# Kernel tuning notes

Hardware: AMD Instinct MI355X
Metric: run time of the kernel (lower is better)

The kernel has to match this reference:

```python
import jax, jax.numpy as jnp
import numpy as np

D_MODEL = 512; D_STATE = 128; D_CONV = 4; EXPAND = 2; HEADDIM = 64; CHUNK = 64
D_INNER = EXPAND * D_MODEL            # 1024
NHEADS = D_INNER // HEADDIM           # 16
CONV_DIM = D_INNER + 2 * D_STATE      # 1280
D_IN_PROJ = 2 * D_INNER + 2 * D_STATE + NHEADS  # 2320
BATCH, SEQLEN = 2, 8192


def setup_inputs() -> dict:
    key = jax.random.key(0)
    ks = jax.random.split(key, 8)
    s = 0.02
    return {
        "x": jax.random.normal(ks[0], (BATCH, SEQLEN, D_MODEL), jnp.float32),
        "in_proj_w": jax.random.normal(ks[1], (D_IN_PROJ, D_MODEL), jnp.float32) * s,
        "conv_w": jax.random.normal(ks[2], (CONV_DIM, 1, D_CONV), jnp.float32) * s,
        "conv_b": jnp.zeros((CONV_DIM,), jnp.float32),
        "dt_bias": jax.random.normal(ks[3], (NHEADS,), jnp.float32) * s,
        "A_log": jnp.log(jnp.arange(1, NHEADS + 1, dtype=jnp.float32)),
        "D_skip": jnp.ones((NHEADS,), jnp.float32),
        "norm_w": jnp.ones((D_INNER,), jnp.float32),
        "ssm_out_w": jax.random.normal(ks[4], (D_MODEL, D_INNER), jnp.float32) * s,
        "fuse_w": jax.random.normal(ks[5], (D_MODEL, 2 * D_MODEL), jnp.float32) * s,
        "fuse_b": jnp.zeros((D_MODEL,), jnp.float32),
    }


def segsum(a):
    # a: (..., T) -> (..., T, T) with [i, j] = sum_{j < d <= i} a[d]; -inf above diag
    T = a.shape[-1]
    a = jnp.broadcast_to(a[..., :, None], a.shape + (T,))
    a = jnp.where(jnp.tril(jnp.ones((T, T), bool), -1), a, 0.0)
    a = jnp.cumsum(a, axis=-2)
    return jnp.where(jnp.tril(jnp.ones((T, T), bool), 0), a, -jnp.inf)


def ssd(x, A, B, C):
    # x: (b,l,h,p), A: (b,l,h), B/C: (b,l,n) (single group, broadcast over heads)
    b, l, h, p = x.shape
    c = l // CHUNK
    x = x.reshape(b, c, CHUNK, h, p)
    A = jnp.transpose(A.reshape(b, c, CHUNK, h), (0, 3, 1, 2))   # (b,h,c,s)
    B = B.reshape(b, c, CHUNK, -1)
    C = C.reshape(b, c, CHUNK, -1)
    A_cumsum = jnp.cumsum(A, axis=-1)                             # (b,h,c,s)
    L = jnp.exp(segsum(A))                                        # (b,h,c,s,s) intra-chunk decay
    Y_diag = jnp.einsum("bcln,bcsn,bhcls,bcshp->bclhp", C, B, L, x)
    decay_states = jnp.exp(A_cumsum[..., -1:] - A_cumsum)         # (b,h,c,s)
    states = jnp.einsum("bcln,bhcl,bclhp->bchpn", B, decay_states, x)
    init = jnp.zeros_like(states[:, :1])
    A_pad = jnp.pad(A_cumsum[..., -1], ((0, 0), (0, 0), (1, 0)))  # (b,h,c+1)
    decay_chunk = jnp.exp(segsum(A_pad))                          # (b,h,c+1,c+1)
    new_states = jnp.einsum("bhzc,bchpn->bzhpn", decay_chunk,
                            jnp.concatenate([init, states], axis=1))
    states = new_states[:, :-1]                                   # state entering each chunk
    state_decay_out = jnp.exp(A_cumsum)
    Y_off = jnp.einsum("bchpn,bcsn,bhcs->bcshp", states, C, state_decay_out)
    return (Y_diag + Y_off).reshape(b, l, h, p)


def mamba2_block(u, in_proj_w, conv_w, conv_b, dt_bias, A_log, D_skip, norm_w, ssm_out_w):
    b, l, _ = u.shape
    zxbcdt = u @ in_proj_w.T                                      # (b,l,2320)
    z = zxbcdt[..., :D_INNER]
    xBC = zxbcdt[..., D_INNER:D_INNER + CONV_DIM]
    dt = jax.nn.softplus(zxbcdt[..., -NHEADS:] + dt_bias)         # (b,l,h)
    # depthwise causal conv over time
    conv = jax.lax.conv_general_dilated(
        jnp.transpose(xBC, (0, 2, 1)), conv_w, (1,), [(D_CONV - 1, 0)],
        dimension_numbers=("NCH", "OIH", "NCH"), feature_group_count=CONV_DIM)
    xBC = jax.nn.silu(jnp.transpose(conv + conv_b[None, :, None], (0, 2, 1)))
    xh = xBC[..., :D_INNER].reshape(b, l, NHEADS, HEADDIM)
    Bm = xBC[..., D_INNER:D_INNER + D_STATE]
    Cm = xBC[..., -D_STATE:]
    A = -jnp.exp(A_log)                                           # (h,)
    y = ssd(xh * dt[..., None], A * dt, Bm, Cm)
    y = y + xh * D_skip[None, None, :, None]
    y = y.reshape(b, l, D_INNER)
    # gated RMSNorm
    y = y * jax.nn.silu(z)
    y = y * jax.lax.rsqrt(jnp.mean(y * y, axis=-1, keepdims=True) + 1e-5) * norm_w
    return y @ ssm_out_w.T


def reference(x, in_proj_w, conv_w, conv_b, dt_bias, A_log, D_skip, norm_w,
              ssm_out_w, fuse_w, fuse_b):
    args = (in_proj_w, conv_w, conv_b, dt_bias, A_log, D_skip, norm_w, ssm_out_w)
    y_fwd = mamba2_block(x, *args)
    y_rev = jnp.flip(mamba2_block(jnp.flip(x, 1), *args), 1)
    y_cat = jnp.concatenate([y_fwd, y_rev], axis=-1)
    return y_cat @ fuse_w.T + fuse_b
```

## Files before the change

### kernel.cpp

```cpp
#include <hip/hip_runtime.h>
#include <cstddef>

#define B_SZ     2
#define L_SEQ    8192
#define D_INNERC 1024
#define NHEADSC  16
#define CHUNKC   64
#define NCHUNKC  128
#define CONV_DIMC 1280
#define D_PROJC  2320
#define M_ROWS   16384

typedef unsigned short bfu;

using bf16x8 = __attribute__((ext_vector_type(8))) short;
using f32x4  = __attribute__((ext_vector_type(4))) float;

__device__ __forceinline__ float silu_(float v) { return v / (1.f + expf(-v)); }

__device__ __forceinline__ float b2f(bfu u) {
  return __uint_as_float((unsigned)u << 16);
}
__device__ __forceinline__ bfu f2b(float f) {
  unsigned x = __float_as_uint(f);
  return (bfu)((x + 0x7fffu + ((x >> 16) & 1u)) >> 16);
}

__device__ __forceinline__ float4 ld4(const float* p) { return *(const float4*)p; }
__device__ __forceinline__ float4 ld4(const bfu* p) {
  ushort4 u = *(const ushort4*)p;
  float4 f;
  f.x = b2f(u.x); f.y = b2f(u.y); f.z = b2f(u.z); f.w = b2f(u.w);
  return f;
}
__device__ __forceinline__ void st4(float* p, float4 v) { *(float4*)p = v; }
__device__ __forceinline__ void st4(bfu* p, float4 v) {
  ushort4 u;
  u.x = f2b(v.x); u.y = f2b(v.y); u.z = f2b(v.z); u.w = f2b(v.w);
  *(ushort4*)p = u;
}

__device__ __forceinline__ void gl_lds16(const bfu* g, bfu* l) {
  __builtin_amdgcn_global_load_lds(
      (const __attribute__((address_space(1))) unsigned int*)g,
      (__attribute__((address_space(3))) unsigned int*)l, 16, 0, 0);
}

__device__ __forceinline__ int pos_of(int b, int c, int l, int dir) {
  int t = c * CHUNKC + l;
  return dir ? (b * L_SEQ + (L_SEQ - 1) - t) : (b * L_SEQ + t);
}

__global__ __launch_bounds__(256)
void mfma_nt(const bfu* __restrict__ A, int lda,
             const bfu* __restrict__ Bw, int ldb,
             void* __restrict__ Cv, int ldc,
             int N, int K, const float* __restrict__ bias, int mode)
{
  __shared__ bfu sh[16384];
  bfu* As = sh;
  bfu* Bs = sh + 8192;
  const int tid  = threadIdx.x;
  const int lane = tid & 63;
  const int wave = __builtin_amdgcn_readfirstlane(tid >> 6);
  const int wm = wave & 1, wn = wave >> 1;

  const int num_n = gridDim.x;
  const int flat  = blockIdx.y * num_n + blockIdx.x;
  const int xcd   = flat & 7;
  const int g     = flat >> 3;
  const int n0 = (g % num_n) * 128;
  const int m0 = ((g / num_n) * 8 + xcd) * 128;

  f32x4 acc[4][4];
#pragma unroll
  for (int i = 0; i < 4; ++i)
#pragma unroll
    for (int j = 0; j < 4; ++j)
      acc[i][j] = (f32x4){0.f, 0.f, 0.f, 0.f};

  const int ro   = lane >> 3;
  const int slot = lane & 7;

  for (int k0 = 0; k0 < K; k0 += 64) {
    __syncthreads();
#pragma unroll
    for (int si = 0; si < 4; ++si) {
      int r = wave * 32 + si * 8 + ro;
      int cg = slot ^ (r & 7);
      gl_lds16(A  + (size_t)(m0 + r) * lda + k0 + cg * 8, As + (wave * 32 + si * 8) * 64);
      gl_lds16(Bw + (size_t)(n0 + r) * ldb + k0 + cg * 8, Bs + (wave * 32 + si * 8) * 64);
    }
    __syncthreads();

#pragma unroll
    for (int ks = 0; ks < 2; ++ks) {
      bf16x8 af[4], bfr[4];
#pragma unroll
      for (int i = 0; i < 4; ++i) {
        int ra = wm * 64 + i * 16 + (lane & 15);
        int ca = (ks * 4 + (lane >> 4)) ^ (ra & 7);
        af[i] = *(const bf16x8*)(As + ra * 64 + ca * 8);
        int rb = wn * 64 + i * 16 + (lane & 15);
        int cb = (ks * 4 + (lane >> 4)) ^ (rb & 7);
        bfr[i] = *(const bf16x8*)(Bs + rb * 64 + cb * 8);
      }
#pragma unroll
      for (int i = 0; i < 4; ++i)
#pragma unroll
        for (int j = 0; j < 4; ++j)
          acc[i][j] = __builtin_amdgcn_mfma_f32_16x16x32_bf16(af[i], bfr[j], acc[i][j], 0, 0, 0);
    }
  }

  __syncthreads();
  if (mode == 0) {
#pragma unroll
    for (int i = 0; i < 4; ++i)
#pragma unroll
      for (int j = 0; j < 4; ++j)
#pragma unroll
        for (int r = 0; r < 4; ++r) {
          int ml = wm * 64 + i * 16 + (lane >> 4) * 4 + r;
          int nl = wn * 64 + j * 16 + (lane & 15);
          sh[ml * 128 + nl] = f2b(acc[i][j][r]);
        }
    __syncthreads();
    bfu* Cb = (bfu*)Cv;
#pragma unroll
    for (int rr = 0; rr < 8; ++rr) {
      int idx = rr * 256 + tid;
      int row = idx >> 4, co = (idx & 15) * 8;
      if (n0 + co < N) {
        *(ulonglong2*)(Cb + (size_t)(m0 + row) * ldc + n0 + co) =
            *(const ulonglong2*)(sh + row * 128 + co);
      }
    }
  } else {
    float* Cf = (float*)Cv;
    float* shf = (float*)sh;
#pragma unroll
    for (int p = 0; p < 2; ++p) {
      if (wm == p) {
#pragma unroll
        for (int i = 0; i < 4; ++i)
#pragma unroll
          for (int j = 0; j < 4; ++j)
#pragma unroll
            for (int r = 0; r < 4; ++r) {
              int ml = i * 16 + (lane >> 4) * 4 + r;
              int nl = wn * 64 + j * 16 + (lane & 15);
              shf[ml * 128 + nl] = acc[i][j][r];
            }
      }
      __syncthreads();
#pragma unroll
      for (int rr = 0; rr < 8; ++rr) {
        int idx = rr * 256 + tid;
        int row = idx >> 5, co = (idx & 31) * 4;
        int n = n0 + co;
        if (n < N) {
          float4 v = *(float4*)(shf + row * 128 + co);
          float* cp = Cf + (size_t)(m0 + p * 64 + row) * ldc + n;
          if (mode == 2) {
            float4 o = *(float4*)cp;
            v.x += o.x; v.y += o.y; v.z += o.z; v.w += o.w;
          } else if (bias) {
            v.x += bias[n]; v.y += bias[n + 1]; v.z += bias[n + 2]; v.w += bias[n + 3];
          }
          *(float4*)cp = v;
        }
      }
      __syncthreads();
    }
  }
}

__global__ __launch_bounds__(256)
void cvt_x_k(const float* __restrict__ in, bfu* __restrict__ out)
{
  int q = blockIdx.x * 256 + threadIdx.x;
  st4(out + (size_t)q * 4, ld4(in + (size_t)q * 4));
}

__global__ __launch_bounds__(256)
void cvt_w_k(const float* __restrict__ in, bfu* __restrict__ out)
{
  int q = blockIdx.x * 256 + threadIdx.x;
  int row = q >> 7, c4 = (q & 127) << 2;
  float4 v = {0.f, 0.f, 0.f, 0.f};
  if (row < D_PROJC) v = ld4(in + (size_t)row * 512 + c4);
  st4(out + (size_t)row * 512 + c4, v);
}

__global__ __launch_bounds__(256)
void transpose_k(const float* __restrict__ in, bfu* __restrict__ out)
{
  int idx = blockIdx.x * 256 + threadIdx.x;
  int j = idx >> 9, k = idx & 511;
  out[idx] = f2b(in[k * 1024 + j]);
}

__global__ __launch_bounds__(256)
void cvt_fuse_k(const float* __restrict__ in, bfu* __restrict__ out)
{
  int q = blockIdx.x * 256 + threadIdx.x;
  int m = q >> 7, kg = (q & 127) << 2;
  float4 v = ld4(in + (size_t)(m & 511) * 1024 + (m >> 9) * 512 + kg);
  st4(out + (size_t)m * 512 + kg, v);
}

__global__ __launch_bounds__(256)
void conv_k(const bfu* __restrict__ zx, const float* __restrict__ conv_w,
            const float* __restrict__ conv_b, bfu* __restrict__ xBC, int dir)
{
  int ch = blockIdx.x * 256 + threadIdx.x;
  int m0 = blockIdx.y * 8;
  int b  = m0 >> 13, tb = m0 & (L_SEQ - 1);
  float w0 = conv_w[ch * 4 + 0], w1 = conv_w[ch * 4 + 1];
  float w2 = conv_w[ch * 4 + 2], w3 = conv_w[ch * 4 + 3];
  float cb = conv_b[ch];
  const bfu* src = zx + 1024 + ch;
  const int shift = dir ? 0 : 3;

  float v[11];
#pragma unroll
  for (int i = 0; i < 11; ++i) {
    int tt = tb + i - shift;
    v[i] = (tt >= 0 && tt < L_SEQ)
         ? b2f(src[(size_t)(b * L_SEQ + tt) * D_PROJC]) : 0.f;
  }
#pragma unroll
  for (int j = 0; j < 8; ++j) {
    float acc = cb;
    if (dir == 0) {
      acc += w0 * v[j] + w1 * v[j + 1] + w2 * v[j + 2] + w3 * v[j + 3];
    } else {
      acc += w0 * v[j + 3] + w1 * v[j + 2] + w2 * v[j + 1] + w3 * v[j];
    }
    xBC[(size_t)(m0 + j) * CONV_DIMC + ch] = f2b(silu_(acc));
  }
}

__global__ __launch_bounds__(256)
void states_mfma_k(const bfu* __restrict__ zx, const bfu* __restrict__ xBC,
                   const float* __restrict__ dt_bias, const float* __restrict__ A_log,
                   float* __restrict__ acum_g, float* __restrict__ dt_g,
                   bfu* __restrict__ states, int dir)
{
  __shared__ bfu BT[128 * 72];
  __shared__ bfu xsT[64 * 72];
  __shared__ float scaleS[8 * 64];

  int bid = blockIdx.x;
  int hb = bid >> 8;
  int c = bid & 127, b = (bid >> 7) & 1;
  int tid = threadIdx.x, lane = tid & 63;
  int w = tid >> 6, q = lane >> 4, t = lane & 15;

#pragma unroll
  for (int rr = 0; rr < 2; ++rr) {
    int i = w + rr * 4;
    int h = hb * 8 + i;
    int l = lane;
    int pos = pos_of(b, c, l, dir);
    float dtr = b2f(zx[(size_t)pos * D_PROJC + 2304 + h]) + dt_bias[h];
    float dt = (dtr > 20.f) ? dtr : log1pf(expf(dtr));
    float a = -expf(A_log[h]) * dt;
#pragma unroll
    for (int off = 1; off < 64; off <<= 1) {
      float v = __shfl_up(a, off);
      if (l >= off) a += v;
    }
    float alast = __shfl(a, 63);
    int gi = ((b * NCHUNKC + c) * NHEADSC + h) * 64 + l;
    acum_g[gi] = a; dt_g[gi] = dt;
    scaleS[i * 64 + l] = dt * expf(alast - a);
  }

#pragma unroll
  for (int r = 0; r < 8; ++r) {
    int qq = tid + r * 256;
    int l = qq & 63, ng = qq >> 6;
    ushort4 v = *(const ushort4*)(xBC + (size_t)pos_of(b, c, l, dir) * CONV_DIMC + 1024 + ng * 4);
    BT[(ng * 4 + 0) * 72 + l] = v.x; BT[(ng * 4 + 1) * 72 + l] = v.y;
    BT[(ng * 4 + 2) * 72 + l] = v.z; BT[(ng * 4 + 3) * 72 + l] = v.w;
  }
  __syncthreads();

  for (int i = 0; i < 8; ++i) {
    int h = hb * 8 + i;
#pragma unroll
    for (int r = 0; r < 4; ++r) {
      int qq = tid + r * 256;
      int l = qq & 63, pg = qq >> 6;
      float s = scaleS[i * 64 + l];
      ushort4 v = *(const ushort4*)(xBC + (size_t)pos_of(b, c, l, dir) * CONV_DIMC + h * 64 + pg * 4);
      xsT[(pg * 4 + 0) * 72 + l] = f2b(b2f(v.x) * s);
      xsT[(pg * 4 + 1) * 72 + l] = f2b(b2f(v.y) * s);
      xsT[(pg * 4 + 2) * 72 + l] = f2b(b2f(v.z) * s);
      xsT[(pg * 4 + 3) * 72 + l] = f2b(b2f(v.w) * s);
    }
    __syncthreads();

    bf16x8 axs[2];
#pragma unroll
    for (int ks = 0; ks < 2; ++ks)
      axs[ks] = *(const bf16x8*)(xsT + (w * 16 + t) * 72 + ks * 32 + q * 8);

    f32x4 acc[8];
#pragma unroll
    for (int j = 0; j < 8; ++j) acc[j] = (f32x4){0.f, 0.f, 0.f, 0.f};
#pragma unroll
    for (int ks = 0; ks < 2; ++ks)
#pragma unroll
      for (int j = 0; j < 8; ++j) {
        bf16x8 bB = *(const bf16x8*)(BT + (j * 16 + t) * 72 + ks * 32 + q * 8);
        acc[j] = __builtin_amdgcn_mfma_f32_16x16x32_bf16(axs[ks], bB, acc[j], 0, 0, 0);
      }

    size_t base = ((size_t)(b * NCHUNKC + c) * NHEADSC + h) * 8192;
#pragma unroll
    for (int j = 0; j < 8; ++j)
#pragma unroll
      for (int r = 0; r < 4; ++r) {
        int p = w * 16 + q * 4 + r, n = j * 16 + t;
        states[base + p * 128 + n] = f2b(acc[j][r]);
      }
    __syncthreads();
  }
}

__global__ __launch_bounds__(256)
void scan_k(bfu* __restrict__ states, const float* __restrict__ acum_g)
{
  int bid = blockIdx.x;
  int eb = bid & 15, h = (bid >> 4) & 15, b = bid >> 8;
  int e = eb * 512 + threadIdx.x * 2;
  bfu* p0 = states + ((size_t)(b * NCHUNKC) * NHEADSC + h) * 8192 + e;
  const float* ac = acum_g + ((b * NCHUNKC) * NHEADSC + h) * 64 + 63;
  const size_t cstride = (size_t)NHEADSC * 8192;
  const int astride = NHEADSC * 64;

  float pre0 = 0.f, pre1 = 0.f;
  uint raw = *(const uint*)p0;
  float dcur = expf(ac[0]);
  for (int c = 0; c < NCHUNKC; ++c) {
    uint raw_next = 0; float dnext = 0.f;
    if (c < NCHUNKC - 1) {
      raw_next = *(const uint*)(p0 + (c + 1) * cstride);
      dnext = expf(ac[(c + 1) * astride]);
    }
    float v0 = b2f((bfu)(raw & 0xffff));
    float v1 = b2f((bfu)(raw >> 16));
    uint packed = (uint)f2b(pre0) | ((uint)f2b(pre1) << 16);
    *(uint*)(p0 + c * cstride) = packed;
    pre0 = v0 + dcur * pre0;
    pre1 = v1 + dcur * pre1;
    raw = raw_next; dcur = dnext;
  }
}

__global__ __launch_bounds__(256)
void y_mfma_k(const bfu* __restrict__ xBC, const bfu* __restrict__ states,
              const float* __restrict__ acum_g, const float* __restrict__ dt_g,
              const float* __restrict__ D_skip, bfu* __restrict__ ybuf, int dir)
{
  __shared__ bfu smem[30976];
  bfu* Cs  = smem;
  bfu* Bsc = smem + 8704;
  bfu* Ps  = smem + 17408;
  bfu* xhT = smem + 26112;
  float* acumH = (float*)(smem + 30720);
  float* dtH   = acumH + 64;

  int bid = blockIdx.x;
  int hb = bid >> 8;
  int c = bid & 127, b = (bid >> 7) & 1;
  int tid = threadIdx.x, lane = tid & 63;
  int w = tid >> 6, q = lane >> 4, t = lane & 15;

#pragma unroll
  for (int r = 0; r < 8; ++r) {
    int qq = tid + r * 256;
    int row = qq >> 5, grp = qq & 31;
    const bfu* src = xBC + (size_t)pos_of(b, c, row, dir) * CONV_DIMC;
    *(ushort4*)(Cs  + row * 136 + grp * 4) = *(const ushort4*)(src + 1152 + grp * 4);
    *(ushort4*)(Bsc + row * 136 + grp * 4) = *(const ushort4*)(src + 1024 + grp * 4);
  }
  __syncthreads();

  bf16x8 af[4];
#pragma unroll
  for (int ks = 0; ks < 4; ++ks)
    af[ks] = *(const bf16x8*)(Cs + (w * 16 + t) * 136 + ks * 32 + q * 8);

  f32x4 sacc[4];
#pragma unroll
  for (int j = 0; j < 4; ++j) sacc[j] = (f32x4){0.f, 0.f, 0.f, 0.f};
#pragma unroll
  for (int ks = 0; ks < 4; ++ks)
#pragma unroll
    for (int j = 0; j < 4; ++j) {
      bf16x8 bf = *(const bf16x8*)(Bsc + (j * 16 + t) * 136 + ks * 32 + q * 8);
      sacc[j] = __builtin_amdgcn_mfma_f32_16x16x32_bf16(af[ks], bf, sacc[j], 0, 0, 0);
    }

  for (int i = 0; i < 8; ++i) {
    int h = hb * 8 + i;
    __syncthreads();
    size_t pbase = ((size_t)(b * NCHUNKC + c) * NHEADSC + h) * 8192;
#pragma unroll
    for (int r = 0; r < 8; ++r) {
      int qq = tid + r * 256;
      int row = qq >> 5, grp = qq & 31;
      *(ushort4*)(Ps + row * 136 + grp * 4) =
          *(const ushort4*)(states + pbase + row * 128 + grp * 4);
    }
#pragma unroll
    for (int r = 0; r < 4; ++r) {
      int qq = tid + r * 256;
      int l = qq & 63, pg = qq >> 6;
      ushort4 v = *(const ushort4*)(xBC + (size_t)pos_of(b, c, l, dir) * CONV_DIMC + h * 64 + pg * 4);
      xhT[(pg * 4 + 0) * 72 + l] = v.x; xhT[(pg * 4 + 1) * 72 + l] = v.y;
      xhT[(pg * 4 + 2) * 72 + l] = v.z; xhT[(pg * 4 + 3) * 72 + l] = v.w;
    }
    if (tid < 64) {
      int gi = ((b * NCHUNKC + c) * NHEADSC + h) * 64 + tid;
      acumH[tid] = acum_g[gi]; dtH[tid] = dt_g[gi];
    }
    __syncthreads();

    f32x4 yacc[4];
#pragma unroll
    for (int j = 0; j < 4; ++j) yacc[j] = (f32x4){0.f, 0.f, 0.f, 0.f};
#pragma unroll
    for (int ks = 0; ks < 4; ++ks)
#pragma unroll
      for (int j = 0; j < 4; ++j) {
        bf16x8 bP = *(const bf16x8*)(Ps + (j * 16 + t) * 136 + ks * 32 + q * 8);
        yacc[j] = __builtin_amdgcn_mfma_f32_16x16x32_bf16(af[ks], bP, yacc[j], 0, 0, 0);
      }

    float Dh = D_skip[h];
    bfu* sc = Bsc;
#pragma unroll
    for (int j = 0; j < 4; ++j)
#pragma unroll
      for (int r = 0; r < 4; ++r) {
        int l = w * 16 + q * 4 + r, s = j * 16 + t;
        float v = 0.f;
        if (s <= l) v = sacc[j][r] * expf(acumH[l] - acumH[s]) * dtH[s];
        if (s == l) v += Dh;
        sc[l * 72 + s] = f2b(v);
      }

    f32x4 acc2[4];
    float dec[4];
#pragma unroll
    for (int r = 0; r < 4; ++r) dec[r] = expf(acumH[w * 16 + q * 4 + r]);
#pragma unroll
    for (int j = 0; j < 4; ++j)
#pragma unroll
      for (int r = 0; r < 4; ++r) acc2[j][r] = yacc[j][r] * dec[r];

#pragma unroll
    for (int ks = 0; ks < 2; ++ks) {
      bf16x8 asc = *(const bf16x8*)(sc + (w * 16 + t) * 72 + ks * 32 + q * 8);
#pragma unroll
      for (int j = 0; j < 4; ++j) {
        bf16x8 bx = *(const bf16x8*)(xhT + (j * 16 + t) * 72 + ks * 32 + q * 8);
        acc2[j] = __builtin_amdgcn_mfma_f32_16x16x32_bf16(asc, bx, acc2[j], 0, 0, 0);
      }
    }

#pragma unroll
    for (int j = 0; j < 4; ++j)
#pragma unroll
      for (int r = 0; r < 4; ++r) {
        int l = w * 16 + q * 4 + r, p = j * 16 + t;
        ybuf[(size_t)pos_of(b, c, l, dir) * D_INNERC + h * 64 + p] = f2b(acc2[j][r]);
      }
  }
}

__global__ __launch_bounds__(256)
void norm_k(bfu* __restrict__ ybuf, const bfu* __restrict__ zx,
            const float* __restrict__ norm_w)
{
  int m = blockIdx.x, tid = threadIdx.x;
  float4 y = ld4(ybuf + (size_t)m * D_INNERC + tid * 4);
  float4 z = ld4(zx + (size_t)m * D_PROJC + tid * 4);
  float4 g;
  g.x = y.x * silu_(z.x); g.y = y.y * silu_(z.y);
  g.z = y.z * silu_(z.z); g.w = y.w * silu_(z.w);
  float ss = g.x * g.x + g.y * g.y + g.z * g.z + g.w * g.w;
#pragma unroll
  for (int off = 32; off >= 1; off >>= 1) ss += __shfl_xor(ss, off);
  __shared__ float red[4];
  int wid = tid >> 6;
  if ((tid & 63) == 0) red[wid] = ss;
  __syncthreads();
  float tot = red[0] + red[1] + red[2] + red[3];
  float scale = rsqrtf(tot * (1.f / 1024.f) + 1e-5f);
  float4 w = *(const float4*)(norm_w + tid * 4);
  g.x *= scale * w.x; g.y *= scale * w.y; g.z *= scale * w.z; g.w *= scale * w.w;
  st4(ybuf + (size_t)m * D_INNERC + tid * 4, g);
}

extern "C" void kernel_launch(void* const* d_in, const int* in_sizes, int n_in,
                              void* d_out, int out_size, void* d_ws, size_t ws_size,
                              hipStream_t stream)
{
  const float* x         = (const float*)d_in[0];
  const float* in_proj_w = (const float*)d_in[1];
  const float* conv_w    = (const float*)d_in[2];
  const float* conv_b    = (const float*)d_in[3];
  const float* dt_bias   = (const float*)d_in[4];
  const float* A_log     = (const float*)d_in[5];
  const float* D_skip    = (const float*)d_in[6];
  const float* norm_w    = (const float*)d_in[7];
  const float* ssm_out_w = (const float*)d_in[8];
  const float* fuse_w    = (const float*)d_in[9];
  const float* fuse_b    = (const float*)d_in[10];
  float* out = (float*)d_out;

  bfu* zx     = (bfu*)d_ws;
  bfu* xBC    = zx     + (size_t)M_ROWS * D_PROJC;
  bfu* states = xBC    + (size_t)M_ROWS * CONV_DIMC;
  bfu* ybuf   = states + (size_t)33554432;
  float* acum = (float*)(ybuf + (size_t)M_ROWS * D_INNERC);
  float* dtg  = acum + 262144;
  bfu* ssmTb  = (bfu*)(dtg + 262144);
  bfu* fuseA  = ssmTb + 524288;
  bfu* wcmb   = fuseA + 524288;
  bfu* xb = states;
  bfu* wb = states + 8388608;

  cvt_x_k<<<8192, 256, 0, stream>>>(x, xb);
  cvt_w_k<<<1216, 256, 0, stream>>>(in_proj_w, wb);
  transpose_k<<<2048, 256, 0, stream>>>(ssm_out_w, ssmTb);
  cvt_fuse_k<<<512, 256, 0, stream>>>(fuse_w, fuseA);

  mfma_nt<<<dim3(8, 8), 256, 0, stream>>>(
      fuseA, 512, ssmTb, 512, wcmb, 1024, 1024, 512, nullptr, 0);

  mfma_nt<<<dim3(19, 128), 256, 0, stream>>>(
      xb, 512, wb, 512, zx, D_PROJC, D_PROJC, 512, nullptr, 0);

  for (int dir = 0; dir < 2; ++dir) {
    conv_k<<<dim3(5, 2048), 256, 0, stream>>>(zx, conv_w, conv_b, xBC, dir);
    states_mfma_k<<<512, 256, 0, stream>>>(zx, xBC, dt_bias, A_log, acum, dtg, states, dir);
    scan_k<<<512, 256, 0, stream>>>(states, acum);
    y_mfma_k<<<512, 256, 0, stream>>>(xBC, states, acum, dtg, D_skip, ybuf, dir);
    norm_k<<<M_ROWS, 256, 0, stream>>>(ybuf, zx, norm_w);
    mfma_nt<<<dim3(4, 128), 256, 0, stream>>>(
        ybuf, 1024, wcmb + (size_t)dir * 524288, 1024, out, 512,
        512, 1024, dir == 0 ? fuse_b : nullptr, dir == 0 ? 1 : 2);
  }
}
```

Before: 528.7 us.

## Add 256x256-tile 8-wave pipelined MFMA GEMM for the input projection

Adds a new 512-thread GEMM kernel with 256x256 output tiles, double-buffered LDS staging via direct global-to-LDS loads, XOR-swizzled layout, and interleaved load/compute phases with explicit waitcnt and barriers. It also remaps blocks across the XCDs. The in_proj GEMM now uses this kernel, and the weight conversion is padded to 2560 rows so the 256-wide N tiles stay in bounds. The aim is more reuse per block and better overlap of memory traffic with MFMA work. In exchange it uses 128KB of LDS and 128 accumulator registers per thread, which limits occupancy, and the last N tile is partly wasted.

```diff
diff --git a/kernel.cpp b/kernel.cpp
--- a/kernel.cpp
+++ b/kernel.cpp
@@ -176,6 +176,157 @@
   }
 }
 
+__global__ __launch_bounds__(512)
+void mfma_nt_8p(const bfu* __restrict__ A, int lda,
+                const bfu* __restrict__ Bw, int ldb,
+                bfu* __restrict__ C, int ldc, int N, int K)
+{
+  __shared__ bfu sh[65536];
+  bfu* As0 = sh;
+  bfu* As1 = sh + 16384;
+  bfu* Bs0 = sh + 32768;
+  bfu* Bs1 = sh + 49152;
+
+  const int tid  = threadIdx.x;
+  const int lane = tid & 63;
+  const int w    = __builtin_amdgcn_readfirstlane(tid >> 6);
+  const int wm = w & 1, wn = w >> 1;
+  const int q = lane >> 4, t = lane & 15;
+
+  const int num_n = gridDim.x;
+  const int flat  = blockIdx.y * num_n + blockIdx.x;
+  const int xcd   = flat & 7;
+  const int g     = flat >> 3;
+  const int n0 = (g % num_n) * 256;
+  const int m0 = ((g / num_n) * 8 + xcd) * 256;
+
+  auto STG = [&](const bfu* __restrict__ X, int ldx, int x0, int kt, int h,
+                 bfu* dst) {
+#pragma unroll
+    for (int ci = 0; ci < 2; ++ci) {
+      int rb = h * 128 + ci * 64 + w * 8;
+      int r  = rb + (lane >> 3);
+      int cg = (lane & 7) ^ (r & 7);
+      gl_lds16(X + (size_t)(x0 + r) * ldx + kt * 64 + cg * 8, dst + rb * 64);
+    }
+  };
+  auto FR = [&](const bfu* tile, int R, int gg) -> bf16x8 {
+    return *(const bf16x8*)(tile + R * 64 + ((gg ^ (R & 7)) * 8));
+  };
+
+  f32x4 acc[8][4];
+#pragma unroll
+  for (int i = 0; i < 8; ++i)
+#pragma unroll
+    for (int j = 0; j < 4; ++j)
+      acc[i][j] = (f32x4){0.f, 0.f, 0.f, 0.f};
+
+  STG(Bw, ldb, n0, 0, 0, Bs0); STG(Bw, ldb, n0, 0, 1, Bs0);
+  STG(A,  lda, m0, 0, 0, As0); STG(A,  lda, m0, 0, 1, As0);
+  STG(Bw, ldb, n0, 1, 0, Bs1); STG(Bw, ldb, n0, 1, 1, Bs1);
+  asm volatile("s_waitcnt vmcnt(4)" ::: "memory");
+  __builtin_amdgcn_s_barrier();
+
+  const int nIter = K >> 7;
+  bf16x8 bfr[4][2];
+  for (int it = 0; it < nIter; ++it) {
+    const int kt = it * 2;
+    const bool last = (it == nIter - 1);
+
+#pragma unroll
+    for (int p = 0; p < 4; ++p) {
+      bf16x8 af[2][2];
+#pragma unroll
+      for (int ii = 0; ii < 2; ++ii)
+#pragma unroll
+        for (int ks = 0; ks < 2; ++ks)
+          af[ii][ks] = FR(As0, wm * 128 + (2 * p + ii) * 16 + t, ks * 4 + q);
+      if (p == 0) {
+#pragma unroll
+        for (int j = 0; j < 4; ++j)
+#pragma unroll
+          for (int ks = 0; ks < 2; ++ks)
+            bfr[j][ks] = FR(Bs0, wn * 64 + j * 16 + t, ks * 4 + q);
+      }
+      if (p == 0)          STG(A,  lda, m0, kt + 1, 0, As1);
+      if (p == 1)          STG(A,  lda, m0, kt + 1, 1, As1);
+      if (p == 2 && !last) STG(Bw, ldb, n0, kt + 2, 0, Bs0);
+      if (p == 3 && !last) STG(Bw, ldb, n0, kt + 2, 1, Bs0);
+      if (p == 3) {
+        if (last) asm volatile("s_waitcnt vmcnt(0)" ::: "memory");
+        else      asm volatile("s_waitcnt vmcnt(4)" ::: "memory");
+      }
+      __builtin_amdgcn_s_barrier();
+      __builtin_amdgcn_s_setprio(1);
+#pragma unroll
+      for (int ks = 0; ks < 2; ++ks)
+#pragma unroll
+        for (int ii = 0; ii < 2; ++ii)
+#pragma unroll
+          for (int j = 0; j < 4; ++j)
+            acc[2 * p + ii][j] = __builtin_amdgcn_mfma_f32_16x16x32_bf16(
+                af[ii][ks], bfr[j][ks], acc[2 * p + ii][j], 0, 0, 0);
+      __builtin_amdgcn_s_setprio(0);
+      __builtin_amdgcn_s_barrier();
+    }
+
+#pragma unroll
+    for (int p = 0; p < 4; ++p) {
+      bf16x8 af[2][2];
+#pragma unroll
+      for (int ii = 0; ii < 2; ++ii)
+#pragma unroll
+        for (int ks = 0; ks < 2; ++ks)
+          af[ii][ks] = FR(As1, wm * 128 + (2 * p + ii) * 16 + t, ks * 4 + q);
+      if (p == 0) {
+#pragma unroll
+        for (int j = 0; j < 4; ++j)
+#pragma unroll
+          for (int ks = 0; ks < 2; ++ks)
+            bfr[j][ks] = FR(Bs1, wn * 64 + j * 16 + t, ks * 4 + q);
+      }
+      if (p == 0 && !last) STG(A,  lda, m0, kt + 2, 0, As0);
+      if (p == 1 && !last) STG(A,  lda, m0, kt + 2, 1, As0);
+      if (p == 2 && !last) STG(Bw, ldb, n0, kt + 3, 0, Bs1);
+      if (p == 3 && !last) STG(Bw, ldb, n0, kt + 3, 1, Bs1);
+      if (p == 3 && !last) asm volatile("s_waitcnt vmcnt(4)" ::: "memory");
+      __builtin_amdgcn_s_barrier();
+      __builtin_amdgcn_s_setprio(1);
+#pragma unroll
+      for (int ks = 0; ks < 2; ++ks)
+#pragma unroll
+        for (int ii = 0; ii < 2; ++ii)
+#pragma unroll
+          for (int j = 0; j < 4; ++j)
+            acc[2 * p + ii][j] = __builtin_amdgcn_mfma_f32_16x16x32_bf16(
+                af[ii][ks], bfr[j][ks], acc[2 * p + ii][j], 0, 0, 0);
+      __builtin_amdgcn_s_setprio(0);
+      __builtin_amdgcn_s_barrier();
+    }
+  }
+
+#pragma unroll
+  for (int i = 0; i < 8; ++i)
+#pragma unroll
+    for (int j = 0; j < 4; ++j)
+#pragma unroll
+      for (int r = 0; r < 4; ++r) {
+        int ml = wm * 128 + i * 16 + q * 4 + r;
+        int nl = wn * 64 + j * 16 + t;
+        sh[ml * 256 + nl] = f2b(acc[i][j][r]);
+      }
+  __syncthreads();
+#pragma unroll
+  for (int rr = 0; rr < 16; ++rr) {
+    int idx = rr * 512 + tid;
+    int row = idx >> 5, co = (idx & 31) * 8;
+    if (n0 + co < N) {
+      *(ulonglong2*)(C + (size_t)(m0 + row) * ldc + n0 + co) =
+          *(const ulonglong2*)(sh + row * 256 + co);
+    }
+  }
+}
+
 __global__ __launch_bounds__(256)
 void cvt_x_k(const float* __restrict__ in, bfu* __restrict__ out)
 {
@@ -538,15 +689,15 @@
   bfu* wb = states + 8388608;
 
   cvt_x_k<<<8192, 256, 0, stream>>>(x, xb);
-  cvt_w_k<<<1216, 256, 0, stream>>>(in_proj_w, wb);
+  cvt_w_k<<<1280, 256, 0, stream>>>(in_proj_w, wb);
   transpose_k<<<2048, 256, 0, stream>>>(ssm_out_w, ssmTb);
   cvt_fuse_k<<<512, 256, 0, stream>>>(fuse_w, fuseA);
 
   mfma_nt<<<dim3(8, 8), 256, 0, stream>>>(
       fuseA, 512, ssmTb, 512, wcmb, 1024, 1024, 512, nullptr, 0);
 
-  mfma_nt<<<dim3(19, 128), 256, 0, stream>>>(
-      xb, 512, wb, 512, zx, D_PROJC, D_PROJC, 512, nullptr, 0);
+  mfma_nt_8p<<<dim3(10, 64), 512, 0, stream>>>(
+      xb, 512, wb, 512, zx, D_PROJC, D_PROJC, 512);
 
   for (int dir = 0; dir < 2; ++dir) {
     conv_k<<<dim3(5, 2048), 256, 0, stream>>>(zx, conv_w, conv_b, xBC, dir);
```

New measurement: 530.0 us. About the same (+0.2%).
